# Kernel tuning notes

Hardware: AMD Instinct MI355X
Metric: run time of the kernel (lower is better)

## Reference

```python
import jax, jax.numpy as jnp
import numpy as np

HIDDEN = 2048
NUM_HEADS = 16
HEAD_DIM = 128
KV_C = 512
Q_C = 1536
ROPE_DIM = 64
B, S = 2, 2048


def _rope(x):
    # x: [B, H, S, D] with D even; interleaved-pair rotation as in the torch module
    b, h, s, d = x.shape
    inv_freq = 1.0 / (10000.0 ** (jnp.arange(0, d, 2, dtype=jnp.float32) / d))  # [d/2]
    pos = jnp.arange(s, dtype=jnp.float32)
    sinusoid = pos[:, None] * inv_freq[None, :]  # [S, d/2]
    sin, cos = jnp.sin(sinusoid), jnp.cos(sinusoid)
    xr = x.reshape(b, h, s, d // 2, 2)
    x1, x2 = xr[..., 0], xr[..., 1]
    out = jnp.stack([x1 * cos - x2 * sin, x1 * sin + x2 * cos], axis=-1)
    return out.reshape(b, h, s, d)


def setup_inputs() -> dict:
    key = jax.random.key(0)
    ks = jax.random.split(key, 12)

    def lin(k, fan_in, fan_out):
        k1, k2 = jax.random.split(k)
        lim = 1.0 / np.sqrt(fan_in)
        w = jax.random.uniform(k1, (fan_in, fan_out), jnp.float32, -lim, lim)
        b = jax.random.uniform(k2, (fan_out,), jnp.float32, -lim, lim)
        return w, b

    kv_down_w, kv_down_b = lin(ks[0], HIDDEN, KV_C)
    key_up_w, key_up_b = lin(ks[1], KV_C, NUM_HEADS * HEAD_DIM)
    value_up_w, value_up_b = lin(ks[2], KV_C, NUM_HEADS * HEAD_DIM)
    key_rope_w, key_rope_b = lin(ks[3], KV_C, NUM_HEADS * ROPE_DIM)
    query_down_w, query_down_b = lin(ks[4], HIDDEN, Q_C)
    query_up_w, query_up_b = lin(ks[5], Q_C, NUM_HEADS * HEAD_DIM)
    query_rope_w, query_rope_b = lin(ks[6], Q_C, NUM_HEADS * ROPE_DIM)
    out_w, out_b = lin(ks[7], NUM_HEADS * HEAD_DIM, HIDDEN)

    x = jax.random.normal(ks[8], (B, S, HIDDEN), jnp.float32)
    attention_mask = jnp.ones((B, S), dtype=jnp.bool_)  # all tokens valid

    return dict(x=x, attention_mask=attention_mask,
                kv_down_w=kv_down_w, kv_down_b=kv_down_b,
                key_up_w=key_up_w, key_up_b=key_up_b,
                value_up_w=value_up_w, value_up_b=value_up_b,
                key_rope_w=key_rope_w, key_rope_b=key_rope_b,
                query_down_w=query_down_w, query_down_b=query_down_b,
                query_up_w=query_up_w, query_up_b=query_up_b,
                query_rope_w=query_rope_w, query_rope_b=query_rope_b,
                out_w=out_w, out_b=out_b)


def reference(x, attention_mask,
              kv_down_w, kv_down_b, key_up_w, key_up_b,
              value_up_w, value_up_b, key_rope_w, key_rope_b,
              query_down_w, query_down_b, query_up_w, query_up_b,
              query_rope_w, query_rope_b, out_w, out_b):
    b, s, _ = x.shape

    kv_c = x @ kv_down_w + kv_down_b                                 # [B,S,KV_C]
    keys_c = (kv_c @ key_up_w + key_up_b).reshape(b, s, NUM_HEADS, HEAD_DIM).transpose(0, 2, 1, 3)
    values = (kv_c @ value_up_w + value_up_b).reshape(b, s, NUM_HEADS, HEAD_DIM).transpose(0, 2, 1, 3)
    keys_r = (kv_c @ key_rope_w + key_rope_b).reshape(b, s, NUM_HEADS, ROPE_DIM).transpose(0, 2, 1, 3)
    keys_r = _rope(keys_r)

    q_c = x @ query_down_w + query_down_b                            # [B,S,Q_C]
    queries_c = (q_c @ query_up_w + query_up_b).reshape(b, s, NUM_HEADS, HEAD_DIM).transpose(0, 2, 1, 3)
    queries_r = (q_c @ query_rope_w + query_rope_b).reshape(b, s, NUM_HEADS, ROPE_DIM).transpose(0, 2, 1, 3)
    queries_r = _rope(queries_r)

    queries = jnp.concatenate([queries_c, queries_r], axis=-1)      # [B,H,S,HD+RD]
    keys = jnp.concatenate([keys_c, keys_r], axis=-1)

    scale = 1.0 / np.sqrt(HEAD_DIM + ROPE_DIM)
    scores = jnp.einsum('bhqd,bhkd->bhqk', queries, keys) * scale   # [B,H,S,S]

    causal = jnp.triu(jnp.ones((s, s), dtype=jnp.bool_), k=1)       # True = masked
    pad = ~attention_mask                                            # [B,S], True = masked key
    mask = causal[None, None, :, :] | pad[:, None, None, :]
    scores = jnp.where(mask, jnp.float32(-1e9), scores)

    probs = jax.nn.softmax(scores, axis=-1)
    context = jnp.einsum('bhqk,bhkd->bhqd', probs, values)          # [B,H,S,HD]
    context = context.transpose(0, 2, 1, 3).reshape(b, s, NUM_HEADS * HEAD_DIM)
    return context @ out_w + out_b                                   # [B,S,HIDDEN]
```

## Files before the change

### kernel.cpp

```cpp
#include <hip/hip_runtime.h>

typedef unsigned short u16;
typedef short short8 __attribute__((ext_vector_type(8)));
typedef short short4v __attribute__((ext_vector_type(4)));
typedef float floatx4 __attribute__((ext_vector_type(4)));
typedef float floatx4v __attribute__((ext_vector_type(4)));

#define SQ 2048
#define NH 16
#define HD 128
#define RD 64
#define NB 2
#define LDKV 5120
#define LDQ 3072

#define LKC 136
#define LKR 72
#define LVT 72
#define LP  72

#define OFF_BC   ((size_t)0)
#define OFF_WT1  ((size_t)16384)
#define OFF_WT2  (OFF_WT1 + (size_t)2048 * 2048)
#define OFF_WT3  (OFF_WT2 + (size_t)5120 * 512)
#define OFF_WTO  (OFF_WT3 + (size_t)3072 * 1536)
#define OFF_KVQD (OFF_WTO + (size_t)2048 * 2048)
#define OFF_KV   (OFF_KVQD + (size_t)4096 * 2048)
#define OFF_QB   (OFF_KV + (size_t)4096 * 5120)

__device__ __forceinline__ float bf2f(u16 u) {
  union { unsigned u; float f; } v; v.u = ((unsigned)u) << 16; return v.f;
}
__device__ __forceinline__ u16 f2bf(float f) {
  union { float f; unsigned u; } v; v.f = f;
  return (u16)((v.u + 0x7FFFu + ((v.u >> 16) & 1u)) >> 16);
}
__device__ __forceinline__ void gll16(const u16* g, u16* l) {
  __builtin_amdgcn_global_load_lds((const __attribute__((address_space(1))) void*)g,
                                   (__attribute__((address_space(3))) void*)l, 16, 0, 0);
}

__global__ __launch_bounds__(256) void prep(
    const float* __restrict__ x,
    const float* b0, const float* b1, const float* b2, const float* b3,
    const float* b4, const float* b5, const float* b6, const float* b7,
    const float* w0, const float* w1, const float* w2, const float* w3,
    const float* w4, const float* w5, const float* w6, const float* w7,
    u16* __restrict__ ws) {
  __shared__ u16 tile[32][33];
  const int blk = blockIdx.x, t = threadIdx.x;

  if (blk < 8192) {
    const int i = blk * 256 + t;
    const floatx4v v = *(const floatx4v*)(x + 4 * (size_t)i);
    short4v o;
    o.x = (short)f2bf(v.x); o.y = (short)f2bf(v.y);
    o.z = (short)f2bf(v.z); o.w = (short)f2bf(v.w);
    *(short4v*)(ws + OFF_QB + 4 * (size_t)i) = o;
    return;
  }
  if (blk < 8240) {
    const int i = (blk - 8192) * 256 + t;
    if (i >= 12288) return;
    float v;
    if      (i < 512)   v = b0[i];
    else if (i < 2048)  v = b1[i - 512];
    else if (i < 4096)  v = b2[i - 2048];
    else if (i < 6144)  v = b3[i - 4096];
    else if (i < 7168)  v = b4[i - 6144];
    else if (i < 9216)  v = b5[i - 7168];
    else if (i < 10240) v = b6[i - 9216];
    else                v = b7[i - 10240];
    ws[OFF_BC + i] = f2bf(v);
    return;
  }
  const int f = blk - 8240;
  const float* in; size_t oo; int R, C, start;
  if      (f < 1024)  { in = w0; oo = OFF_WT1;                        R = 2048; C = 512;  start = 0; }
  else if (f < 4096)  { in = w1; oo = OFF_WT1 + (size_t)512 * 2048;   R = 2048; C = 1536; start = 1024; }
  else if (f < 5120)  { in = w2; oo = OFF_WT2;                        R = 512;  C = 2048; start = 4096; }
  else if (f < 6144)  { in = w3; oo = OFF_WT2 + (size_t)2048 * 512;   R = 512;  C = 2048; start = 5120; }
  else if (f < 6656)  { in = w4; oo = OFF_WT2 + (size_t)4096 * 512;   R = 512;  C = 1024; start = 6144; }
  else if (f < 9728)  { in = w5; oo = OFF_WT3;                        R = 1536; C = 2048; start = 6656; }
  else if (f < 11264) { in = w6; oo = OFF_WT3 + (size_t)2048 * 1536;  R = 1536; C = 1024; start = 9728; }
  else                { in = w7; oo = OFF_WTO;                        R = 2048; C = 2048; start = 11264; }
  u16* out = ws + oo;
  const int local = f - start, nx = C / 32;
  const int c0 = (local % nx) * 32, r0 = (local / nx) * 32;
  const int xx = t & 31, y = t >> 5;
#pragma unroll
  for (int i = 0; i < 32; i += 8)
    tile[y + i][xx] = f2bf(in[(size_t)(r0 + y + i) * C + c0 + xx]);
  __syncthreads();
#pragma unroll
  for (int i = 0; i < 32; i += 8)
    out[(size_t)(c0 + y + i) * R + r0 + xx] = tile[xx][y + i];
}

__global__ __launch_bounds__(256) void post(u16* __restrict__ ws) {
  __shared__ u16 tile[32][33];
  const int blk = blockIdx.x, t = threadIdx.x;

  if (blk < 16384) {
    u16* buf; int ld, coloff, f;
    if (blk < 8192) { buf = ws + OFF_KV; ld = LDKV; coloff = 4096; f = blk; }
    else            { buf = ws + OFF_QB; ld = LDQ;  coloff = 2048; f = blk - 8192; }
    const int i = f * 256 + t;
    const int j = i & 31;
    const int hh = (i >> 5) & 15;
    const int row = i >> 9;
    const int s = row & (SQ - 1);
    u16* p = buf + (size_t)row * ld + coloff + hh * RD + 2 * j;
    const float x1 = bf2f(p[0]), x2 = bf2f(p[1]);
    const float inv = exp2f(-(float)j * 0.41524101186092031f);
    const float ang = (float)s * inv;
    float sn, cs;
    sincosf(ang, &sn, &cs);
    p[0] = f2bf(x1 * cs - x2 * sn);
    p[1] = f2bf(x1 * sn + x2 * cs);
    return;
  }
  const int f = blk - 16384;
  const int bh = f >> 8, rem = f & 255;
  const int b = bh >> 4, hh = bh & 15;
  const int s0 = (rem & 63) * 32, d0 = (rem >> 6) * 32;
  const u16* pin = ws + OFF_KV + (size_t)b * SQ * LDKV + 2048 + (size_t)hh * HD;
  u16* pout = ws + OFF_KVQD + (size_t)bh * HD * SQ;
  const int xx = t & 31, y = t >> 5;
#pragma unroll
  for (int i = 0; i < 32; i += 8)
    tile[y + i][xx] = pin[(size_t)(s0 + y + i) * LDKV + d0 + xx];
  __syncthreads();
#pragma unroll
  for (int i = 0; i < 32; i += 8)
    pout[(size_t)(d0 + y + i) * SQ + s0 + xx] = tile[xx][y + i];
}

__global__ __launch_bounds__(512, 4) void gemm_bt(const u16* __restrict__ A, int lda,
                                                  const u16* __restrict__ Bt,
                                                  const u16* __restrict__ bias,
                                                  void* __restrict__ Cout, int ldc,
                                                  int wf32, int N, int K) {
  __shared__ __align__(16) u16 lAk0[128 * 32];
  __shared__ __align__(16) u16 lAk1[128 * 32];
  __shared__ __align__(16) u16 lBk0[128 * 32];
  __shared__ __align__(16) u16 lBk1[128 * 32];
  const int t = threadIdx.x;
  const int lane = t & 63, w = t >> 6;
  const int wm = w & 1, wn = w >> 1;
  const int m0 = blockIdx.y * 128, n0 = blockIdx.x * 128;
  const int srow = t >> 2, scol = (t & 3) * 8;
  const u16* gA = A + (size_t)(m0 + srow) * lda + scol;
  const u16* gB = Bt + (size_t)(n0 + srow) * K + scol;
  u16* const ldA0 = lAk0 + (16 * w) * 32;
  u16* const ldA1 = lAk1 + (16 * w) * 32;
  u16* const ldB0 = lBk0 + (16 * w) * 32;
  u16* const ldB1 = lBk1 + (16 * w) * 32;
  const int lane_m = lane & 15, lane_k = (lane >> 4) * 8;
  floatx4 acc[4][2] = {};
  for (int k0 = 0; k0 < K; k0 += 64) {
    gll16(gA + k0, ldA0);
    gll16(gA + k0 + 32, ldA1);
    gll16(gB + k0, ldB0);
    gll16(gB + k0 + 32, ldB1);
    __syncthreads();
    {
      short8 af[4], bf[2];
#pragma unroll
      for (int i = 0; i < 4; i++)
        af[i] = *(const short8*)(lAk0 + (wm * 64 + i * 16 + lane_m) * 32 + lane_k);
#pragma unroll
      for (int i = 0; i < 2; i++)
        bf[i] = *(const short8*)(lBk0 + (wn * 32 + i * 16 + lane_m) * 32 + lane_k);
#pragma unroll
      for (int mi = 0; mi < 4; mi++)
#pragma unroll
        for (int ni = 0; ni < 2; ni++)
          acc[mi][ni] = __builtin_amdgcn_mfma_f32_16x16x32_bf16(af[mi], bf[ni], acc[mi][ni], 0, 0, 0);
    }
    {
      short8 af[4], bf[2];
#pragma unroll
      for (int i = 0; i < 4; i++)
        af[i] = *(const short8*)(lAk1 + (wm * 64 + i * 16 + lane_m) * 32 + lane_k);
#pragma unroll
      for (int i = 0; i < 2; i++)
        bf[i] = *(const short8*)(lBk1 + (wn * 32 + i * 16 + lane_m) * 32 + lane_k);
#pragma unroll
      for (int mi = 0; mi < 4; mi++)
#pragma unroll
        for (int ni = 0; ni < 2; ni++)
          acc[mi][ni] = __builtin_amdgcn_mfma_f32_16x16x32_bf16(af[mi], bf[ni], acc[mi][ni], 0, 0, 0);
    }
    __syncthreads();
  }
  const int quad = lane >> 4;
#pragma unroll
  for (int ni = 0; ni < 2; ni++) {
    const int col = n0 + wn * 32 + ni * 16 + lane_m;
    const float bv = bf2f(bias[col]);
#pragma unroll
    for (int mi = 0; mi < 4; mi++) {
      const int row = m0 + wm * 64 + mi * 16 + quad * 4;
      if (wf32) {
        float* pc = (float*)Cout + (size_t)row * ldc + col;
#pragma unroll
        for (int r = 0; r < 4; r++)
          pc[(size_t)r * ldc] = acc[mi][ni][r] + bv;
      } else {
        u16* pc = (u16*)Cout + (size_t)row * ldc + col;
#pragma unroll
        for (int r = 0; r < 4; r++)
          pc[(size_t)r * ldc] = f2bf(acc[mi][ni][r] + bv);
      }
    }
  }
}

__global__ __launch_bounds__(512, 4) void flash_attn(const u16* __restrict__ Q,
                                                     const u16* __restrict__ KV,
                                                     const u16* __restrict__ Vt,
                                                     u16* __restrict__ Ctx) {
  __shared__ __align__(16) u16 lKc[64 * LKC];
  __shared__ __align__(16) u16 lKr[64 * LKR];
  __shared__ __align__(16) u16 lVt[128 * LVT];
  __shared__ __align__(16) u16 lP[8 * 16 * LP];
  const int t = threadIdx.x, lane = t & 63, w = t >> 6;
  const int col = blockIdx.y;
  const int qtile = (col < 16) ? (15 - (int)blockIdx.x) : (int)blockIdx.x;
  const int h = col & (NH - 1);
  const int b = col >> 4;
  const int q0 = qtile * 128;
  const int nkt = 2 * qtile + 2;
  const int lane_m = lane & 15, quad = lane >> 4, lane_k = quad * 8;

  const int qrow = q0 + 16 * w + lane_m;
  const u16* qcp = Q + (size_t)(b * SQ + qrow) * LDQ + h * HD;
  const u16* qrp = Q + (size_t)(b * SQ + qrow) * LDQ + 2048 + h * RD;
  short8 qfc[4], qfr[2];
#pragma unroll
  for (int ks = 0; ks < 4; ks++) qfc[ks] = *(const short8*)(qcp + ks * 32 + lane_k);
#pragma unroll
  for (int ks = 0; ks < 2; ks++) qfr[ks] = *(const short8*)(qrp + ks * 32 + lane_k);

  floatx4 O[8] = {};
  float mrow[4], lsum[4];
#pragma unroll
  for (int r = 0; r < 4; r++) { mrow[r] = -1e30f; lsum[r] = 0.f; }

  const u16* gKc = KV + (size_t)b * SQ * LDKV + h * HD;
  const u16* gKr = KV + (size_t)b * SQ * LDKV + 4096 + h * RD;
  const u16* gVt = Vt + (size_t)(b * NH + h) * HD * SQ;
  const float C2 = 0.10412825525540364f;
  const float THR = 28.8f;

  short8 rKc[2], rKr, rVt[2];
  auto load_tile = [&](int kb) {
#pragma unroll
    for (int i = 0; i < 2; i++) {
      const int c = t + i * 512, row = c >> 4, cc = (c & 15) * 8;
      rKc[i] = *(const short8*)(gKc + (size_t)(kb + row) * LDKV + cc);
    }
    {
      const int row = t >> 3, cc = (t & 7) * 8;
      rKr = *(const short8*)(gKr + (size_t)(kb + row) * LDKV + cc);
    }
#pragma unroll
    for (int i = 0; i < 2; i++) {
      const int c = t + i * 512, row = c >> 3, cc = (c & 7) * 8;
      rVt[i] = *(const short8*)(gVt + (size_t)row * SQ + kb + cc);
    }
  };

  const int wrow_lo = q0 + 16 * w;
  const int wrow_hi = wrow_lo + 15;

  load_tile(0);
  for (int kt = 0; kt < nkt; kt++) {
    const int kb = kt * 64;
    __syncthreads();
#pragma unroll
    for (int i = 0; i < 2; i++) {
      const int c = t + i * 512, row = c >> 4, cc = (c & 15) * 8;
      *(short8*)(lKc + row * LKC + cc) = rKc[i];
    }
    {
      const int row = t >> 3, cc = (t & 7) * 8;
      *(short8*)(lKr + row * LKR + cc) = rKr;
    }
#pragma unroll
    for (int i = 0; i < 2; i++) {
      const int c = t + i * 512, row = c >> 3, cc = (c & 7) * 8;
      *(short8*)(lVt + row * LVT + cc) = rVt[i];
    }
    __syncthreads();
    if (kt < nkt - 1) load_tile(kb + 64);

    if (kb <= wrow_hi) {
      float ss[4][4];
      __builtin_amdgcn_s_setprio(1);
#pragma unroll
      for (int n = 0; n < 4; n++) {
        floatx4 a = {0.f, 0.f, 0.f, 0.f};
#pragma unroll
        for (int ks = 0; ks < 4; ks++) {
          const short8 kf = *(const short8*)(lKc + (n * 16 + lane_m) * LKC + ks * 32 + lane_k);
          a = __builtin_amdgcn_mfma_f32_16x16x32_bf16(qfc[ks], kf, a, 0, 0, 0);
        }
#pragma unroll
        for (int ks = 0; ks < 2; ks++) {
          const short8 kf = *(const short8*)(lKr + (n * 16 + lane_m) * LKR + ks * 32 + lane_k);
          a = __builtin_amdgcn_mfma_f32_16x16x32_bf16(qfr[ks], kf, a, 0, 0, 0);
        }
#pragma unroll
        for (int r = 0; r < 4; r++) ss[n][r] = a[r];
      }
      __builtin_amdgcn_s_setprio(0);
      if (kb + 63 > wrow_lo) {
#pragma unroll
        for (int n = 0; n < 4; n++) {
          const int kcol = kb + n * 16 + lane_m;
#pragma unroll
          for (int r = 0; r < 4; r++) {
            const int row = wrow_lo + quad * 4 + r;
            if (kcol > row) ss[n][r] = -1e30f;
          }
        }
      }
      float mt[4];
#pragma unroll
      for (int r = 0; r < 4; r++) {
        float m = fmaxf(fmaxf(ss[0][r], ss[1][r]), fmaxf(ss[2][r], ss[3][r]));
#pragma unroll
        for (int d = 1; d < 16; d <<= 1) m = fmaxf(m, __shfl_xor(m, d));
        mt[r] = m;
      }
      const bool grow = (mt[0] > mrow[0] + THR) || (mt[1] > mrow[1] + THR) ||
                        (mt[2] > mrow[2] + THR) || (mt[3] > mrow[3] + THR);
      if (__any(grow)) {
#pragma unroll
        for (int r = 0; r < 4; r++) {
          const float mn = fmaxf(mrow[r], mt[r]);
          const float alpha = exp2f((mrow[r] - mn) * C2);
          mrow[r] = mn;
          lsum[r] *= alpha;
#pragma unroll
          for (int vb = 0; vb < 8; vb++) O[vb][r] *= alpha;
        }
      }
      float pw[4][4];
#pragma unroll
      for (int r = 0; r < 4; r++) {
        float s = 0.f;
#pragma unroll
        for (int n = 0; n < 4; n++) {
          const float p = exp2f((ss[n][r] - mrow[r]) * C2);
          pw[n][r] = p;
          s += p;
        }
#pragma unroll
        for (int d = 1; d < 16; d <<= 1) s += __shfl_xor(s, d);
        lsum[r] += s;
      }
#pragma unroll
      for (int n = 0; n < 4; n++)
#pragma unroll
        for (int r = 0; r < 4; r++)
          lP[(w * 16 + quad * 4 + r) * LP + n * 16 + lane_m] = f2bf(pw[n][r]);
      asm volatile("s_waitcnt lgkmcnt(0)" ::: "memory");
      __builtin_amdgcn_s_setprio(1);
#pragma unroll
      for (int ks = 0; ks < 2; ks++) {
        const short8 pf = *(const short8*)(lP + (w * 16 + lane_m) * LP + ks * 32 + lane_k);
#pragma unroll
        for (int vb = 0; vb < 8; vb++) {
          const short8 vf = *(const short8*)(lVt + (vb * 16 + lane_m) * LVT + ks * 32 + lane_k);
          O[vb] = __builtin_amdgcn_mfma_f32_16x16x32_bf16(pf, vf, O[vb], 0, 0, 0);
        }
      }
      __builtin_amdgcn_s_setprio(0);
    }
  }
  float inv[4];
#pragma unroll
  for (int r = 0; r < 4; r++) inv[r] = 1.f / lsum[r];
#pragma unroll
  for (int vb = 0; vb < 8; vb++) {
#pragma unroll
    for (int r = 0; r < 4; r++) {
      const int row = wrow_lo + quad * 4 + r;
      Ctx[(size_t)(b * SQ + row) * 2048 + h * HD + vb * 16 + lane_m] = f2bf(O[vb][r] * inv[r]);
    }
  }
}

extern "C" void kernel_launch(void* const* d_in, const int* in_sizes, int n_in,
                              void* d_out, int out_size, void* d_ws, size_t ws_size,
                              hipStream_t stream) {
  (void)in_sizes; (void)n_in; (void)out_size; (void)ws_size;
  const float* x    = (const float*)d_in[0];
  const float* kvdw = (const float*)d_in[2];
  const float* kvdb = (const float*)d_in[3];
  const float* kuw  = (const float*)d_in[4];
  const float* kub  = (const float*)d_in[5];
  const float* vuw  = (const float*)d_in[6];
  const float* vub  = (const float*)d_in[7];
  const float* krw  = (const float*)d_in[8];
  const float* krb  = (const float*)d_in[9];
  const float* qdw  = (const float*)d_in[10];
  const float* qdb  = (const float*)d_in[11];
  const float* quw  = (const float*)d_in[12];
  const float* qub  = (const float*)d_in[13];
  const float* qrw  = (const float*)d_in[14];
  const float* qrb  = (const float*)d_in[15];
  const float* ow   = (const float*)d_in[16];
  const float* ob   = (const float*)d_in[17];

  u16* ws   = (u16*)d_ws;
  u16* bc   = ws + OFF_BC;
  u16* WT1  = ws + OFF_WT1;
  u16* WT2  = ws + OFF_WT2;
  u16* WT3  = ws + OFF_WT3;
  u16* WTo  = ws + OFF_WTO;
  u16* KVQd = ws + OFF_KVQD;
  u16* KV   = ws + OFF_KV;
  u16* Qb   = ws + OFF_QB;
  u16* Ctx  = WT1;
  u16* Vt   = KVQd;
  u16* xc   = Qb;

  prep<<<dim3(23600), 256, 0, stream>>>(x, kvdb, qdb, kub, vub, krb, qub, qrb, ob,
                                        kvdw, qdw, kuw, vuw, krw, quw, qrw, ow, ws);

  auto G = [&](const u16* A, int lda, const u16* Bt, const u16* bias,
               void* Cout, int ldc, int wf32, int N, int K) {
    gemm_bt<<<dim3(N / 128, 4096 / 128), 512, 0, stream>>>(A, lda, Bt, bias, Cout, ldc, wf32, N, K);
  };
  G(xc, 2048, WT1, bc, KVQd, 2048, 0, 2048, 2048);
  G(KVQd, 2048, WT2, bc + 2048, KV, LDKV, 0, 5120, 512);
  G(KVQd + 512, 2048, WT3, bc + 7168, Qb, LDQ, 0, 3072, 1536);

  post<<<dim3(24576), 256, 0, stream>>>(ws);

  flash_attn<<<dim3(16, 32), 512, 0, stream>>>(Qb, KV, Vt, Ctx);

  G(Ctx, 2048, WTo, bc + 10240, d_out, 2048, 1, 2048, 2048);
}
```

Baseline: 505.2 us.

## Merge KV and Q up-projection GEMMs into one launch; fuse query RoPE into attention

The gemm kernel now takes two problem descriptors and a split index, so the KV up-projection and the Q up-projection run as one 1D-grid launch, filling the GPU better and removing a launch. The query RoPE pass is dropped from the post kernel and applied in registers when flash attention loads its query fragments. This removes one kernel launch and a read/write pass over the query rope columns. In exchange, each attention block recomputes sincos for its query rows.

```diff
diff --git a/kernel.cpp b/kernel.cpp
--- a/kernel.cpp
+++ b/kernel.cpp
@@ -101,16 +101,14 @@
   __shared__ u16 tile[32][33];
   const int blk = blockIdx.x, t = threadIdx.x;
 
-  if (blk < 16384) {
-    u16* buf; int ld, coloff, f;
-    if (blk < 8192) { buf = ws + OFF_KV; ld = LDKV; coloff = 4096; f = blk; }
-    else            { buf = ws + OFF_QB; ld = LDQ;  coloff = 2048; f = blk - 8192; }
-    const int i = f * 256 + t;
+  if (blk < 8192) {
+    u16* buf = ws + OFF_KV;
+    const int i = blk * 256 + t;
     const int j = i & 31;
     const int hh = (i >> 5) & 15;
     const int row = i >> 9;
     const int s = row & (SQ - 1);
-    u16* p = buf + (size_t)row * ld + coloff + hh * RD + 2 * j;
+    u16* p = buf + (size_t)row * LDKV + 4096 + hh * RD + 2 * j;
     const float x1 = bf2f(p[0]), x2 = bf2f(p[1]);
     const float inv = exp2f(-(float)j * 0.41524101186092031f);
     const float ang = (float)s * inv;
@@ -120,7 +118,7 @@
     p[1] = f2bf(x1 * sn + x2 * cs);
     return;
   }
-  const int f = blk - 16384;
+  const int f = blk - 8192;
   const int bh = f >> 8, rem = f & 255;
   const int b = bh >> 4, hh = bh & 15;
   const int s0 = (rem & 63) * 32, d0 = (rem >> 6) * 32;
@@ -136,19 +134,29 @@
     pout[(size_t)(d0 + y + i) * SQ + s0 + xx] = tile[xx][y + i];
 }
 
-__global__ __launch_bounds__(512, 4) void gemm_bt(const u16* __restrict__ A, int lda,
-                                                  const u16* __restrict__ Bt,
-                                                  const u16* __restrict__ bias,
-                                                  void* __restrict__ Cout, int ldc,
-                                                  int wf32, int N, int K) {
+__global__ __launch_bounds__(512, 4) void gemm_bt(
+    int split,
+    const u16* __restrict__ A1, int lda1, const u16* __restrict__ B1,
+    const u16* __restrict__ bias1, void* __restrict__ C1, int ldc1, int wf1, int N1, int K1,
+    const u16* __restrict__ A2, int lda2, const u16* __restrict__ B2,
+    const u16* __restrict__ bias2, void* __restrict__ C2, int ldc2, int wf2, int N2, int K2) {
   __shared__ __align__(16) u16 lAk0[128 * 32];
   __shared__ __align__(16) u16 lAk1[128 * 32];
   __shared__ __align__(16) u16 lBk0[128 * 32];
   __shared__ __align__(16) u16 lBk1[128 * 32];
+  int id = blockIdx.x;
+  const u16 *A, *Bt, *bias; void* Cout; int lda, ldc, wf32, N, K;
+  if (id < split) {
+    A = A1; lda = lda1; Bt = B1; bias = bias1; Cout = C1; ldc = ldc1; wf32 = wf1; N = N1; K = K1;
+  } else {
+    id -= split;
+    A = A2; lda = lda2; Bt = B2; bias = bias2; Cout = C2; ldc = ldc2; wf32 = wf2; N = N2; K = K2;
+  }
+  const int nx = N >> 7;
+  const int m0 = (id / nx) * 128, n0 = (id % nx) * 128;
   const int t = threadIdx.x;
   const int lane = t & 63, w = t >> 6;
   const int wm = w & 1, wn = w >> 1;
-  const int m0 = blockIdx.y * 128, n0 = blockIdx.x * 128;
   const int srow = t >> 2, scol = (t & 3) * 8;
   const u16* gA = A + (size_t)(m0 + srow) * lda + scol;
   const u16* gB = Bt + (size_t)(n0 + srow) * K + scol;
@@ -240,8 +248,24 @@
   short8 qfc[4], qfr[2];
 #pragma unroll
   for (int ks = 0; ks < 4; ks++) qfc[ks] = *(const short8*)(qcp + ks * 32 + lane_k);
-#pragma unroll
-  for (int ks = 0; ks < 2; ks++) qfr[ks] = *(const short8*)(qrp + ks * 32 + lane_k);
+  {
+    const float sp = (float)qrow;
+#pragma unroll
+    for (int ks = 0; ks < 2; ks++) {
+      short8 v = *(const short8*)(qrp + ks * 32 + lane_k);
+#pragma unroll
+      for (int p = 0; p < 4; p++) {
+        const int j = ks * 16 + quad * 4 + p;
+        const float inv = exp2f(-(float)j * 0.41524101186092031f);
+        float sn, cs;
+        sincosf(sp * inv, &sn, &cs);
+        const float x1 = bf2f((u16)v[2 * p]), x2 = bf2f((u16)v[2 * p + 1]);
+        v[2 * p]     = (short)f2bf(x1 * cs - x2 * sn);
+        v[2 * p + 1] = (short)f2bf(x1 * sn + x2 * cs);
+      }
+      qfr[ks] = v;
+    }
+  }
 
   floatx4 O[8] = {};
   float mrow[4], lsum[4];
@@ -428,21 +452,24 @@
   u16* Ctx  = WT1;
   u16* Vt   = KVQd;
   u16* xc   = Qb;
+  const u16* nu = (const u16*)nullptr;
 
   prep<<<dim3(23600), 256, 0, stream>>>(x, kvdb, qdb, kub, vub, krb, qub, qrb, ob,
                                         kvdw, qdw, kuw, vuw, krw, quw, qrw, ow, ws);
 
-  auto G = [&](const u16* A, int lda, const u16* Bt, const u16* bias,
-               void* Cout, int ldc, int wf32, int N, int K) {
-    gemm_bt<<<dim3(N / 128, 4096 / 128), 512, 0, stream>>>(A, lda, Bt, bias, Cout, ldc, wf32, N, K);
-  };
-  G(xc, 2048, WT1, bc, KVQd, 2048, 0, 2048, 2048);
-  G(KVQd, 2048, WT2, bc + 2048, KV, LDKV, 0, 5120, 512);
-  G(KVQd + 512, 2048, WT3, bc + 7168, Qb, LDQ, 0, 3072, 1536);
-
-  post<<<dim3(24576), 256, 0, stream>>>(ws);
+  gemm_bt<<<dim3(512), 512, 0, stream>>>(1 << 30,
+      xc, 2048, WT1, bc, KVQd, 2048, 0, 2048, 2048,
+      nu, 0, nu, nu, (void*)nullptr, 0, 0, 0, 64);
+
+  gemm_bt<<<dim3(2048), 512, 0, stream>>>(1280,
+      KVQd, 2048, WT2, bc + 2048, KV, LDKV, 0, 5120, 512,
+      KVQd + 512, 2048, WT3, bc + 7168, Qb, LDQ, 0, 3072, 1536);
+
+  post<<<dim3(16384), 256, 0, stream>>>(ws);
 
   flash_attn<<<dim3(16, 32), 512, 0, stream>>>(Qb, KV, Vt, Ctx);
 
-  G(Ctx, 2048, WTo, bc + 10240, d_out, 2048, 1, 2048, 2048);
-}
+  gemm_bt<<<dim3(512), 512, 0, stream>>>(1 << 30,
+      Ctx, 2048, WTo, bc + 10240, d_out, 2048, 1, 2048, 2048,
+      nu, 0, nu, nu, (void*)nullptr, 0, 0, 0, 64);
+}
```

New measurement: 471.7 us. 6.6% less time.
